# Kernel tuning notes

Measured on AMD Instinct MI355X. Metric: run time of the kernel, lower is better.

The kernel has to match this reference:

```python
import jax, jax.numpy as jnp
import numpy as np

K = 3          # kernel size
STRIDE = 1
PAD = 1
GROUPS = 32    # GroupNorm groups
EPS = 1e-5


def setup_inputs() -> dict:
    key = jax.random.key(0)
    ks = jax.random.split(key, 6)
    B, Cin, H, W, Cout = 4, 256, 64, 64, 256
    K2 = K * K
    x = jax.random.normal(ks[0], (B, Cin, H, W), jnp.float32)
    offset = jax.random.normal(ks[1], (B, 2 * K2, H, W), jnp.float32)
    mask = jax.random.uniform(ks[2], (B, K2, H, W), jnp.float32)
    weight = jax.random.normal(ks[3], (Cout, Cin, K, K), jnp.float32) * (1.0 / np.sqrt(Cin * K2))
    bias = jnp.zeros((Cout,), jnp.float32)
    gamma = jnp.ones((Cout,), jnp.float32)   # constant_init(norm, 1)
    beta = jnp.zeros((Cout,), jnp.float32)   # bias=0
    return {"x": x, "offset": offset, "mask": mask, "weight": weight,
            "bias": bias, "gamma": gamma, "beta": beta}


def _modulated_deform_conv(x, offset, mask, weight, bias):
    """DCNv2: bilinear-sample x at learned offsets, modulate by mask, conv-accumulate."""
    B, Cin, H, W = x.shape
    Cout = weight.shape[0]
    K2 = K * K
    Ho = (H + 2 * PAD - K) // STRIDE + 1
    Wo = (W + 2 * PAD - K) // STRIDE + 1

    # base sampling grid per kernel point: [K2, Ho, Wo]
    ky, kx = jnp.meshgrid(jnp.arange(K), jnp.arange(K), indexing='ij')
    ky = ky.reshape(K2).astype(jnp.float32)
    kx = kx.reshape(K2).astype(jnp.float32)
    hs = (jnp.arange(Ho) * STRIDE - PAD).astype(jnp.float32)
    ws = (jnp.arange(Wo) * STRIDE - PAD).astype(jnp.float32)

    off = offset.reshape(B, K2, 2, Ho, Wo)  # interleaved (dy, dx) per kernel point
    y = ky[None, :, None, None] + hs[None, None, :, None] + off[:, :, 0]   # [B,K2,Ho,Wo]
    xc = kx[None, :, None, None] + ws[None, None, None, :] + off[:, :, 1]  # [B,K2,Ho,Wo]

    y0 = jnp.floor(y)
    x0 = jnp.floor(xc)
    dy = y - y0
    dx = xc - x0
    y0i = y0.astype(jnp.int32)
    x0i = x0.astype(jnp.int32)

    x_flat = x.reshape(B, Cin, H * W)

    def corner(yi, xi, w):
        # corner-wise zero padding outside the image (matches mmcv bilinear)
        valid = (yi >= 0) & (yi <= H - 1) & (xi >= 0) & (xi <= W - 1)
        idx = jnp.clip(yi, 0, H - 1) * W + jnp.clip(xi, 0, W - 1)  # [B,K2,Ho,Wo]
        idx_f = idx.reshape(B, -1)
        v = jax.vmap(lambda xf, i: xf[:, i])(x_flat, idx_f)  # [B, Cin, K2*Ho*Wo]
        wv = (w * valid.astype(w.dtype)).reshape(B, 1, -1)
        return v * wv

    val = (corner(y0i,     x0i,     (1 - dy) * (1 - dx))
         + corner(y0i,     x0i + 1, (1 - dy) * dx)
         + corner(y0i + 1, x0i,     dy * (1 - dx))
         + corner(y0i + 1, x0i + 1, dy * dx))
    val = val.reshape(B, Cin, K2, Ho, Wo) * mask[:, None]  # modulate

    w_r = weight.reshape(Cout, Cin, K2)
    out = jnp.einsum('bckhw,ock->bohw', val, w_r) + bias[None, :, None, None]
    return out


def _group_norm(x, gamma, beta):
    B, C, H, W = x.shape
    g = x.reshape(B, GROUPS, C // GROUPS, H, W)
    mu = g.mean(axis=(2, 3, 4), keepdims=True)
    var = ((g - mu) ** 2).mean(axis=(2, 3, 4), keepdims=True)
    g = (g - mu) * jax.lax.rsqrt(var + EPS)
    return g.reshape(B, C, H, W) * gamma[None, :, None, None] + beta[None, :, None, None]


def reference(x, offset, mask, weight, bias, gamma, beta):
    out = _modulated_deform_conv(x, offset, mask, weight, bias)
    out = _group_norm(out, gamma, beta)
    return jax.nn.relu(out)
```

## Files before the change

kernel.cpp:

```cpp
#include <hip/hip_runtime.h>
#include <math.h>

#define BB    4
#define CIN   256
#define HH    64
#define WWID  64
#define COUT  256
#define KKS   3
#define K2    9
#define PADV  1
#define HWSZ  4096
#define GROUPS 32
#define CPG   8
#define EPSV  1e-5f
#define ROWB  4608
#define NKC   36

typedef __attribute__((ext_vector_type(8))) short bf16x8;
typedef __attribute__((ext_vector_type(4))) float f32x4;
typedef __attribute__((ext_vector_type(2))) float f32x2;

#define GLOAD_LDS16(g, l) \
    __builtin_amdgcn_global_load_lds((const __attribute__((address_space(1))) unsigned int*)(g), \
                                     (__attribute__((address_space(3))) unsigned int*)(l), 16, 0, 0)

__device__ __forceinline__ unsigned short f2bf(float f) {
    unsigned u = __float_as_uint(f);
    u = (u + 0x7fffu + ((u >> 16) & 1u)) >> 16;
    return (unsigned short)u;
}
__device__ __forceinline__ f32x2 up2(unsigned q) {
    f32x2 v;
    v.x = __uint_as_float(q << 16);
    v.y = __uint_as_float(q & 0xffff0000u);
    return v;
}
__device__ __forceinline__ unsigned cvtpk(f32x2 f) {
    unsigned r;
    asm("v_cvt_pk_bf16_f32 %0, %1, %2" : "=v"(r) : "v"(f.x), "v"(f.y));
    return r;
}

__global__ __launch_bounds__(256)
void k_pre(const float* __restrict__ x, unsigned short* __restrict__ xh,
           const float* __restrict__ w, unsigned short* __restrict__ wtb,
           float* __restrict__ gstat) {
    int t = threadIdx.x;
    if (blockIdx.x < 128) {
        __shared__ float tile[32][33];
        int hw0 = blockIdx.x * 32;
        int c0  = blockIdx.y * 32;
        int b   = blockIdx.z;
        int tx = t & 31, ty = t >> 5;
        const float* xp = x + (size_t)b * CIN * HWSZ;
        #pragma unroll
        for (int i = 0; i < 4; i++)
            tile[ty + i * 8][tx] = xp[(c0 + ty + i * 8) * HWSZ + hw0 + tx];
        __syncthreads();
        int j = t >> 3, cq = t & 7;
        union { unsigned short s[4]; uint2 d; } pk;
        #pragma unroll
        for (int k = 0; k < 4; k++) pk.s[k] = f2bf(tile[cq * 4 + k][j]);
        *(uint2*)((char*)xh + ((size_t)b * HWSZ * CIN + (size_t)(hw0 + j) * CIN + c0 + cq * 4) * 2) = pk.d;
    } else {
        if (blockIdx.y == 0 && blockIdx.z == 0)
            for (int i = t; i < BB * GROUPS * 2 + 8; i += 256) gstat[i] = 0.f;
        int idx = (blockIdx.y * 4 + blockIdx.z) * 256 + t;
        int co = idx >> 5, c8 = idx & 31;
        int cin0 = c8 * 8;
        int q = c8 >> 3, c = c8 & 7;
        int pc = c ^ (co & 7);
        for (int k2 = 0; k2 < K2; k2++) {
            union { unsigned short s[8]; uint4 qq; } pk;
            #pragma unroll
            for (int j = 0; j < 8; j++)
                pk.s[j] = f2bf(w[(co * CIN + cin0 + j) * K2 + k2]);
            int phys = co * ROWB + k2 * 512 + q * 128 + pc * 16;
            *(uint4*)((char*)wtb + phys) = pk.qq;
        }
    }
}

__global__ __launch_bounds__(256)
void k_conv(const unsigned short* __restrict__ wtb, const unsigned short* __restrict__ xh,
            const float* __restrict__ offset, const float* __restrict__ mask,
            const float* __restrict__ bias, float* __restrict__ out,
            float* __restrict__ gstat) {
    __shared__ __align__(16) unsigned short As[256 * 64];
    __shared__ __align__(16) unsigned short Bs[32 * 64];
    __shared__ __align__(16) int   cidx[32 * K2 * 4];
    __shared__ __align__(16) float cwgt[32 * K2 * 4];
    __shared__ float gs[32], gss[32];

    int lid = blockIdx.x;
    int strip = (lid & 7) * 64 + (lid >> 3);
    int b = strip >> 7;
    int hwbase = (strip & 127) * 32;

    int t = threadIdx.x, w = t >> 6, l = t & 63;
    int r16 = l & 15, hf = l >> 4;
    int skey = r16 & 7;

    if (t < 32) { gs[t] = 0.f; gss[t] = 0.f; }

    for (int i = t; i < 32 * K2; i += 256) {
        int px = i / K2, k2 = i - px * K2;
        int hw = hwbase + px;
        int ho = hw >> 6, wo = hw & 63;
        int ky = k2 / KKS, kx = k2 - ky * KKS;
        float dy = offset[((b * (2 * K2) + k2 * 2 + 0) * HWSZ) + hw];
        float dx = offset[((b * (2 * K2) + k2 * 2 + 1) * HWSZ) + hw];
        float m  = mask[(b * K2 + k2) * HWSZ + hw];
        float y  = (float)(ky + ho - PADV) + dy;
        float xc = (float)(kx + wo - PADV) + dx;
        float y0f = floorf(y), x0f = floorf(xc);
        float fy = y - y0f, fx = xc - x0f;
        int y0 = (int)y0f, x0 = (int)x0f;
        int   yy[2] = { y0, y0 + 1 };
        int   xx[2] = { x0, x0 + 1 };
        float wy[2] = { 1.f - fy, fy };
        float wx[2] = { 1.f - fx, fx };
        #pragma unroll
        for (int ii = 0; ii < 2; ii++)
            #pragma unroll
            for (int jj = 0; jj < 2; jj++) {
                int yi = yy[ii], xi = xx[jj];
                bool valid = (yi >= 0) && (yi < HH) && (xi >= 0) && (xi < WWID);
                int yc  = min(max(yi, 0), HH - 1);
                int xcc = min(max(xi, 0), WWID - 1);
                cidx[i * 4 + ii * 2 + jj] = (yc * WWID + xcc) << 9;
                cwgt[i * 4 + ii * 2 + jj] = valid ? (wy[ii] * wx[jj] * m) : 0.f;
            }
    }

    const char* agb = (const char*)wtb + (size_t)(t >> 3) * ROWB + (t & 7) * 16;
    unsigned short* lA = (unsigned short*)As + t * 8;

    int sc  = t & 7;
    int px0 = t >> 3;
    const char* xb = (const char*)xh + (size_t)b * HWSZ * CIN * 2 + sc * 16;
    int bofs0 = px0 * 64 + (sc ^ (px0 & 7)) * 8;

    f32x4 acc[4][2];
    #pragma unroll
    for (int mi = 0; mi < 4; mi++)
        #pragma unroll
        for (int ni = 0; ni < 2; ni++) acc[mi][ni] = (f32x4)0.f;

    __syncthreads();

    uint4 g[4]; float gw[4];
    {
        int cb = (px0 * K2) * 4;
        int4   ci = *(const int4*)&cidx[cb];
        float4 cw = *(const float4*)&cwgt[cb];
        gw[0] = cw.x; gw[1] = cw.y; gw[2] = cw.z; gw[3] = cw.w;
        g[0] = *(const uint4*)(xb + ci.x);
        g[1] = *(const uint4*)(xb + ci.y);
        g[2] = *(const uint4*)(xb + ci.z);
        g[3] = *(const uint4*)(xb + ci.w);
    }

    for (int kc = 0; kc < NKC; kc++) {
        #pragma unroll
        for (int i = 0; i < 8; i++)
            GLOAD_LDS16(agb + (size_t)i * (32 * (size_t)ROWB), lA + i * 2048);
        agb += 128;

        {
            f32x2 f0 = {0.f, 0.f}, f1 = {0.f, 0.f}, f2 = {0.f, 0.f}, f3 = {0.f, 0.f};
            #pragma unroll
            for (int c = 0; c < 4; c++) {
                f32x2 wv = { gw[c], gw[c] };
                f0 = __builtin_elementwise_fma(wv, up2(g[c].x), f0);
                f1 = __builtin_elementwise_fma(wv, up2(g[c].y), f1);
                f2 = __builtin_elementwise_fma(wv, up2(g[c].z), f2);
                f3 = __builtin_elementwise_fma(wv, up2(g[c].w), f3);
            }
            uint4 pk;
            pk.x = cvtpk(f0); pk.y = cvtpk(f1); pk.z = cvtpk(f2); pk.w = cvtpk(f3);
            *(uint4*)&Bs[bofs0] = pk;
        }
        __syncthreads();

        if (kc < NKC - 1) {
            int kn = kc + 1;
            int k2n = kn >> 2, qn = kn & 3;
            int cb = (px0 * K2 + k2n) * 4;
            int4   ci = *(const int4*)&cidx[cb];
            float4 cw = *(const float4*)&cwgt[cb];
            gw[0] = cw.x; gw[1] = cw.y; gw[2] = cw.z; gw[3] = cw.w;
            const char* xq = xb + qn * 128;
            g[0] = *(const uint4*)(xq + ci.x);
            g[1] = *(const uint4*)(xq + ci.y);
            g[2] = *(const uint4*)(xq + ci.z);
            g[3] = *(const uint4*)(xq + ci.w);
        }

        #pragma unroll
        for (int ks = 0; ks < 2; ks++) {
            int up = ((ks * 4 + hf) ^ skey) * 8;
            bf16x8 af[4], bv[2];
            #pragma unroll
            for (int mi = 0; mi < 4; mi++)
                af[mi] = *(const bf16x8*)&As[(w * 64 + mi * 16 + r16) * 64 + up];
            #pragma unroll
            for (int ni = 0; ni < 2; ni++)
                bv[ni] = *(const bf16x8*)&Bs[(ni * 16 + r16) * 64 + up];
            #pragma unroll
            for (int mi = 0; mi < 4; mi++)
                #pragma unroll
                for (int ni = 0; ni < 2; ni++)
                    acc[mi][ni] = __builtin_amdgcn_mfma_f32_16x16x32_bf16(
                        af[mi], bv[ni], acc[mi][ni], 0, 0, 0);
        }
        __syncthreads();
    }

    float s4[4] = {0,0,0,0}, ss4[4] = {0,0,0,0};
    #pragma unroll
    for (int mi = 0; mi < 4; mi++) {
        #pragma unroll
        for (int r = 0; r < 4; r++) {
            int co = w * 64 + mi * 16 + hf * 4 + r;
            float bs = bias[co];
            float* orow = out + ((size_t)(b * COUT + co)) * HWSZ;
            #pragma unroll
            for (int ni = 0; ni < 2; ni++) {
                int n = hwbase + ni * 16 + r16;
                float v = acc[mi][ni][r] + bs;
                orow[n] = v;
                s4[mi] += v; ss4[mi] += v * v;
            }
        }
    }
    int gb = hf >> 1;
    #pragma unroll
    for (int mi = 0; mi < 4; mi++) {
        atomicAdd(&gs [w * 8 + mi * 2 + gb], s4[mi]);
        atomicAdd(&gss[w * 8 + mi * 2 + gb], ss4[mi]);
    }
    __syncthreads();
    if (t < 32) {
        atomicAdd(&gstat[(b * GROUPS + t) * 2 + 0], gs[t]);
        atomicAdd(&gstat[(b * GROUPS + t) * 2 + 1], gss[t]);
    }
}

__global__ __launch_bounds__(256)
void k_gnfinal(float* __restrict__ out, const float* __restrict__ gstat,
               const float* __restrict__ gamma, const float* __restrict__ beta) {
    int i4 = blockIdx.x * 256 + threadIdx.x;
    int e  = i4 * 4;
    int c  = (e >> 12) & 255;
    int b  = e >> 20;
    int g  = c >> 3;
    float s  = gstat[((b * GROUPS) + g) * 2 + 0];
    float ss = gstat[((b * GROUPS) + g) * 2 + 1];
    const float inv = 1.f / (float)(CPG * HWSZ);
    float mu  = s * inv;
    float var = ss * inv - mu * mu;
    float rstd = rsqrtf(var + EPSV);
    float ga = gamma[c] * rstd;
    float be = beta[c] - mu * ga;
    float4 v = ((float4*)out)[i4];
    v.x = fmaxf(v.x * ga + be, 0.f);
    v.y = fmaxf(v.y * ga + be, 0.f);
    v.z = fmaxf(v.z * ga + be, 0.f);
    v.w = fmaxf(v.w * ga + be, 0.f);
    ((float4*)out)[i4] = v;
}

extern "C" void kernel_launch(void* const* d_in, const int* in_sizes, int n_in,
                              void* d_out, int out_size, void* d_ws, size_t ws_size,
                              hipStream_t stream) {
    const float* x      = (const float*)d_in[0];
    const float* offset = (const float*)d_in[1];
    const float* mask   = (const float*)d_in[2];
    const float* weight = (const float*)d_in[3];
    const float* bias   = (const float*)d_in[4];
    const float* gamma  = (const float*)d_in[5];
    const float* beta   = (const float*)d_in[6];
    float* out = (float*)d_out;

    unsigned short* xh    = (unsigned short*)d_ws;
    unsigned short* wtb   = xh + (size_t)4194304;
    float*          gstat = (float*)(wtb + (size_t)589824);

    k_pre<<<dim3(129, 8, 4), 256, 0, stream>>>(x, xh, weight, wtb, gstat);
    k_conv<<<512, 256, 0, stream>>>(wtb, xh, offset, mask, bias, out, gstat);
    k_gnfinal<<<(size_t)BB * COUT * HWSZ / 1024, 256, 0, stream>>>(out, gstat, gamma, beta);
}
```

Measured before the change: 154.4 us.

## Double-buffer conv tiles, widen block to 64 pixels with 512 threads

The deformable conv GEMM kernel now uses 512-thread blocks covering 64 output pixels, so each staged weight tile is reused across twice as many pixels. A/B shared-memory tiles are double-buffered, which lets the next weight stage and bilinear gather be issued before the current MFMA step and cuts one barrier per K-chunk. MFMA sections are raised in priority with s_setprio. In exchange the block uses much more LDS (about 80KB), and there are half as many blocks (256), which may hurt occupancy and load balance.

```diff
diff --git a/kernel.cpp b/kernel.cpp
--- a/kernel.cpp
+++ b/kernel.cpp
@@ -81,29 +81,100 @@
     }
 }
 
-__global__ __launch_bounds__(256)
+#define STAGE(dst) do { \
+    _Pragma("unroll") \
+    for (int i_ = 0; i_ < 4; i_++) \
+        GLOAD_LDS16(agb + (size_t)i_ * (64 * (size_t)ROWB), (dst) + i_ * 4096); \
+    agb += 128; \
+} while (0)
+
+#define GATHER(kn) do { \
+    int k2n_ = (kn) >> 2, qn_ = (kn) & 3; \
+    int cb_ = (px0 * K2 + k2n_) * 4; \
+    int4   ci_ = *(const int4*)&cidx[cb_]; \
+    float4 cw_ = *(const float4*)&cwgt[cb_]; \
+    gw[0] = cw_.x; gw[1] = cw_.y; gw[2] = cw_.z; gw[3] = cw_.w; \
+    const char* xq_ = xb + qn_ * 128; \
+    g[0] = *(const uint4*)(xq_ + ci_.x); \
+    g[1] = *(const uint4*)(xq_ + ci_.y); \
+    g[2] = *(const uint4*)(xq_ + ci_.z); \
+    g[3] = *(const uint4*)(xq_ + ci_.w); \
+} while (0)
+
+#define PACK(Bdst) do { \
+    f32x2 f0 = {0.f, 0.f}, f1 = {0.f, 0.f}, f2 = {0.f, 0.f}, f3 = {0.f, 0.f}; \
+    _Pragma("unroll") \
+    for (int c_ = 0; c_ < 4; c_++) { \
+        f32x2 wv_ = { gw[c_], gw[c_] }; \
+        f0 = __builtin_elementwise_fma(wv_, up2(g[c_].x), f0); \
+        f1 = __builtin_elementwise_fma(wv_, up2(g[c_].y), f1); \
+        f2 = __builtin_elementwise_fma(wv_, up2(g[c_].z), f2); \
+        f3 = __builtin_elementwise_fma(wv_, up2(g[c_].w), f3); \
+    } \
+    uint4 pk_; \
+    pk_.x = cvtpk(f0); pk_.y = cvtpk(f1); pk_.z = cvtpk(f2); pk_.w = cvtpk(f3); \
+    *(uint4*)&(Bdst)[bofs0] = pk_; \
+} while (0)
+
+#define MFMA_STEP(Ac, Bc) do { \
+    __builtin_amdgcn_s_setprio(1); \
+    _Pragma("unroll") \
+    for (int ks_ = 0; ks_ < 2; ks_++) { \
+        int up_ = ((ks_ * 4 + hf) ^ skey) * 8; \
+        bf16x8 af_[4], bv_[2]; \
+        _Pragma("unroll") \
+        for (int mi_ = 0; mi_ < 4; mi_++) \
+            af_[mi_] = *(const bf16x8*)&(Ac)[(wm * 64 + mi_ * 16 + r16) * 64 + up_]; \
+        _Pragma("unroll") \
+        for (int ni_ = 0; ni_ < 2; ni_++) \
+            bv_[ni_] = *(const bf16x8*)&(Bc)[(wn * 32 + ni_ * 16 + r16) * 64 + up_]; \
+        _Pragma("unroll") \
+        for (int mi_ = 0; mi_ < 4; mi_++) \
+            _Pragma("unroll") \
+            for (int ni_ = 0; ni_ < 2; ni_++) \
+                acc[mi_][ni_] = __builtin_amdgcn_mfma_f32_16x16x32_bf16( \
+                    af_[mi_], bv_[ni_], acc[mi_][ni_], 0, 0, 0); \
+    } \
+    __builtin_amdgcn_s_setprio(0); \
+} while (0)
+
+#define BODY(kc, Ac, An, Bc, Bn, lAn) do { \
+    if ((kc) + 1 < NKC) { \
+        STAGE(lAn); \
+        GATHER((kc) + 1); \
+        __builtin_amdgcn_sched_barrier(0); \
+    } \
+    MFMA_STEP(Ac, Bc); \
+    if ((kc) + 1 < NKC) { \
+        PACK(Bn); \
+        __syncthreads(); \
+    } \
+} while (0)
+
+__global__ __launch_bounds__(512, 2)
 void k_conv(const unsigned short* __restrict__ wtb, const unsigned short* __restrict__ xh,
             const float* __restrict__ offset, const float* __restrict__ mask,
             const float* __restrict__ bias, float* __restrict__ out,
             float* __restrict__ gstat) {
-    __shared__ __align__(16) unsigned short As[256 * 64];
-    __shared__ __align__(16) unsigned short Bs[32 * 64];
-    __shared__ __align__(16) int   cidx[32 * K2 * 4];
-    __shared__ __align__(16) float cwgt[32 * K2 * 4];
+    __shared__ __align__(16) unsigned short As[2][256 * 64];
+    __shared__ __align__(16) unsigned short Bs[2][64 * 64];
+    __shared__ __align__(16) int   cidx[64 * K2 * 4];
+    __shared__ __align__(16) float cwgt[64 * K2 * 4];
     __shared__ float gs[32], gss[32];
 
     int lid = blockIdx.x;
-    int strip = (lid & 7) * 64 + (lid >> 3);
-    int b = strip >> 7;
-    int hwbase = (strip & 127) * 32;
+    int strip = (lid & 7) * 32 + (lid >> 3);
+    int b = strip >> 6;
+    int hwbase = (strip & 63) * 64;
 
     int t = threadIdx.x, w = t >> 6, l = t & 63;
     int r16 = l & 15, hf = l >> 4;
     int skey = r16 & 7;
+    int wm = w & 3, wn = w >> 2;
 
     if (t < 32) { gs[t] = 0.f; gss[t] = 0.f; }
 
-    for (int i = t; i < 32 * K2; i += 256) {
+    for (int i = t; i < 64 * K2; i += 512) {
         int px = i / K2, k2 = i - px * K2;
         int hw = hwbase + px;
         int ho = hw >> 6, wo = hw & 63;
@@ -134,7 +205,8 @@
     }
 
     const char* agb = (const char*)wtb + (size_t)(t >> 3) * ROWB + (t & 7) * 16;
-    unsigned short* lA = (unsigned short*)As + t * 8;
+    unsigned short* lA0 = &As[0][t * 8];
+    unsigned short* lA1 = &As[1][t * 8];
 
     int sc  = t & 7;
     int px0 = t >> 3;
@@ -150,71 +222,14 @@
     __syncthreads();
 
     uint4 g[4]; float gw[4];
-    {
-        int cb = (px0 * K2) * 4;
-        int4   ci = *(const int4*)&cidx[cb];
-        float4 cw = *(const float4*)&cwgt[cb];
-        gw[0] = cw.x; gw[1] = cw.y; gw[2] = cw.z; gw[3] = cw.w;
-        g[0] = *(const uint4*)(xb + ci.x);
-        g[1] = *(const uint4*)(xb + ci.y);
-        g[2] = *(const uint4*)(xb + ci.z);
-        g[3] = *(const uint4*)(xb + ci.w);
-    }
-
-    for (int kc = 0; kc < NKC; kc++) {
-        #pragma unroll
-        for (int i = 0; i < 8; i++)
-            GLOAD_LDS16(agb + (size_t)i * (32 * (size_t)ROWB), lA + i * 2048);
-        agb += 128;
-
-        {
-            f32x2 f0 = {0.f, 0.f}, f1 = {0.f, 0.f}, f2 = {0.f, 0.f}, f3 = {0.f, 0.f};
-            #pragma unroll
-            for (int c = 0; c < 4; c++) {
-                f32x2 wv = { gw[c], gw[c] };
-                f0 = __builtin_elementwise_fma(wv, up2(g[c].x), f0);
-                f1 = __builtin_elementwise_fma(wv, up2(g[c].y), f1);
-                f2 = __builtin_elementwise_fma(wv, up2(g[c].z), f2);
-                f3 = __builtin_elementwise_fma(wv, up2(g[c].w), f3);
-            }
-            uint4 pk;
-            pk.x = cvtpk(f0); pk.y = cvtpk(f1); pk.z = cvtpk(f2); pk.w = cvtpk(f3);
-            *(uint4*)&Bs[bofs0] = pk;
-        }
-        __syncthreads();
-
-        if (kc < NKC - 1) {
-            int kn = kc + 1;
-            int k2n = kn >> 2, qn = kn & 3;
-            int cb = (px0 * K2 + k2n) * 4;
-            int4   ci = *(const int4*)&cidx[cb];
-            float4 cw = *(const float4*)&cwgt[cb];
-            gw[0] = cw.x; gw[1] = cw.y; gw[2] = cw.z; gw[3] = cw.w;
-            const char* xq = xb + qn * 128;
-            g[0] = *(const uint4*)(xq + ci.x);
-            g[1] = *(const uint4*)(xq + ci.y);
-            g[2] = *(const uint4*)(xq + ci.z);
-            g[3] = *(const uint4*)(xq + ci.w);
-        }
-
-        #pragma unroll
-        for (int ks = 0; ks < 2; ks++) {
-            int up = ((ks * 4 + hf) ^ skey) * 8;
-            bf16x8 af[4], bv[2];
-            #pragma unroll
-            for (int mi = 0; mi < 4; mi++)
-                af[mi] = *(const bf16x8*)&As[(w * 64 + mi * 16 + r16) * 64 + up];
-            #pragma unroll
-            for (int ni = 0; ni < 2; ni++)
-                bv[ni] = *(const bf16x8*)&Bs[(ni * 16 + r16) * 64 + up];
-            #pragma unroll
-            for (int mi = 0; mi < 4; mi++)
-                #pragma unroll
-                for (int ni = 0; ni < 2; ni++)
-                    acc[mi][ni] = __builtin_amdgcn_mfma_f32_16x16x32_bf16(
-                        af[mi], bv[ni], acc[mi][ni], 0, 0, 0);
-        }
-        __syncthreads();
+    GATHER(0);
+    STAGE(lA0);
+    PACK(Bs[0]);
+    __syncthreads();
+
+    for (int kc2 = 0; kc2 < NKC; kc2 += 2) {
+        BODY(kc2,     As[0], As[1], Bs[0], Bs[1], lA1);
+        BODY(kc2 + 1, As[1], As[0], Bs[1], Bs[0], lA0);
     }
 
     float s4[4] = {0,0,0,0}, ss4[4] = {0,0,0,0};
@@ -222,12 +237,12 @@
     for (int mi = 0; mi < 4; mi++) {
         #pragma unroll
         for (int r = 0; r < 4; r++) {
-            int co = w * 64 + mi * 16 + hf * 4 + r;
+            int co = wm * 64 + mi * 16 + hf * 4 + r;
             float bs = bias[co];
             float* orow = out + ((size_t)(b * COUT + co)) * HWSZ;
             #pragma unroll
             for (int ni = 0; ni < 2; ni++) {
-                int n = hwbase + ni * 16 + r16;
+                int n = hwbase + wn * 32 + ni * 16 + r16;
                 float v = acc[mi][ni][r] + bs;
                 orow[n] = v;
                 s4[mi] += v; ss4[mi] += v * v;
@@ -237,8 +252,8 @@
     int gb = hf >> 1;
     #pragma unroll
     for (int mi = 0; mi < 4; mi++) {
-        atomicAdd(&gs [w * 8 + mi * 2 + gb], s4[mi]);
-        atomicAdd(&gss[w * 8 + mi * 2 + gb], ss4[mi]);
+        atomicAdd(&gs [wm * 8 + mi * 2 + gb], s4[mi]);
+        atomicAdd(&gss[wm * 8 + mi * 2 + gb], ss4[mi]);
     }
     __syncthreads();
     if (t < 32) {
@@ -288,6 +303,6 @@
     float*          gstat = (float*)(wtb + (size_t)589824);
 
     k_pre<<<dim3(129, 8, 4), 256, 0, stream>>>(x, xh, weight, wtb, gstat);
-    k_conv<<<512, 256, 0, stream>>>(wtb, xh, offset, mask, bias, out, gstat);
+    k_conv<<<256, 512, 0, stream>>>(wtb, xh, offset, mask, bias, out, gstat);
     k_gnfinal<<<(size_t)BB * COUT * HWSZ / 1024, 256, 0, stream>>>(out, gstat, gamma, beta);
 }
```

New measurement: 152.0 us. No clear change (-1.6%).
